# Kernel tuning notes

Hardware: AMD Instinct MI355X
Metric: run time of the kernel (lower is better)

## Reference

```python
import jax, jax.numpy as jnp
import numpy as np

TOKENS, D_MODEL, FC1, FC2 = 4096, 4096, 16384, 4096
EPS = 1e-3


def setup_inputs() -> dict:
    key = jax.random.key(0)
    ks = jax.random.split(key, 3)
    return {
        "inputs": jax.random.normal(ks[0], (TOKENS, D_MODEL), dtype=jnp.float32),
        "gamma": jnp.ones((D_MODEL,), dtype=jnp.float32),
        "beta": jnp.zeros((D_MODEL,), dtype=jnp.float32),
        "fc1_kernel": jax.random.normal(ks[1], (D_MODEL, FC1), dtype=jnp.float32) * 0.023,
        "fc1_bias": jnp.zeros((FC1,), dtype=jnp.float32),
        "fc2_kernel": jax.random.normal(ks[2], (FC1, FC2), dtype=jnp.float32) * 0.023,
        "fc2_bias": jnp.zeros((FC2,), dtype=jnp.float32),
    }


def _layernorm(x, gamma, beta):
    mu = jnp.mean(x, axis=-1, keepdims=True)
    var = jnp.mean(jnp.square(x - mu), axis=-1, keepdims=True)
    rsigma = jax.lax.rsqrt(var + EPS)
    return (x - mu) * rsigma * gamma + beta


def _gelu_tanh(x):
    # gelu with approximate=True (tanh approximation)
    c = jnp.asarray(0.7978845608028654, x.dtype)  # sqrt(2/pi)
    return 0.5 * x * (1.0 + jnp.tanh(c * (x + 0.044715 * x * x * x)))


def reference(inputs, gamma, beta, fc1_kernel, fc1_bias, fc2_kernel, fc2_bias):
    ln_out = _layernorm(inputs, gamma, beta)            # [T, D]
    fc1_out = jnp.matmul(ln_out, fc1_kernel) + fc1_bias  # [T, FC1]
    gelu_out = _gelu_tanh(fc1_out)
    fc2_out = jnp.matmul(gelu_out, fc2_kernel) + fc2_bias  # [T, FC2]
    return fc2_out
```

## Files before the change

### kernel.cpp

```cpp
#include <hip/hip_runtime.h>
#include <stdint.h>

#define TOKENS 4096
#define DMODEL 4096
#define FC1N   16384
#define FC2N   4096

typedef __attribute__((ext_vector_type(8))) __bf16 bf16x8;
typedef __attribute__((ext_vector_type(4))) float f32x4;

__device__ __forceinline__ unsigned short f2bf(float f) {
  unsigned u = __float_as_uint(f);
  u += 0x7fffu + ((u >> 16) & 1u);
  return (unsigned short)(u >> 16);
}

__device__ __forceinline__ float gelu_tanh(float x) {
  float y = 0.7978845608028654f * (x + 0.044715f * x * x * x);
  float e = __expf(2.0f * y);
  float t = 1.0f - 2.0f / (e + 1.0f);
  return 0.5f * x * (1.0f + t);
}

__global__ __launch_bounds__(256) void ln_kernel(const float* __restrict__ x,
                                                 const float* __restrict__ gamma,
                                                 const float* __restrict__ beta,
                                                 unsigned short* __restrict__ out) {
  const int row = blockIdx.x;
  const int tid = threadIdx.x;
  const float* xr = x + (size_t)row * DMODEL;
  float4 v[4];
  float s = 0.f, s2 = 0.f;
#pragma unroll
  for (int i = 0; i < 4; ++i) {
    v[i] = ((const float4*)xr)[tid + i * 256];
    s  += v[i].x + v[i].y + v[i].z + v[i].w;
    s2 += v[i].x * v[i].x + v[i].y * v[i].y + v[i].z * v[i].z + v[i].w * v[i].w;
  }
#pragma unroll
  for (int o = 32; o > 0; o >>= 1) {
    s  += __shfl_xor(s, o, 64);
    s2 += __shfl_xor(s2, o, 64);
  }
  __shared__ float red[2][4];
  const int wid = tid >> 6, lane = tid & 63;
  if (lane == 0) { red[0][wid] = s; red[1][wid] = s2; }
  __syncthreads();
  s  = red[0][0] + red[0][1] + red[0][2] + red[0][3];
  s2 = red[1][0] + red[1][1] + red[1][2] + red[1][3];
  const float mu = s * (1.f / DMODEL);
  const float var = s2 * (1.f / DMODEL) - mu * mu;
  const float rs = rsqrtf(var + 1e-3f);
  unsigned short* orow = out + (size_t)row * DMODEL;
#pragma unroll
  for (int i = 0; i < 4; ++i) {
    const int c4 = tid + i * 256;
    float4 g = ((const float4*)gamma)[c4];
    float4 b = ((const float4*)beta)[c4];
    ushort4 o;
    o.x = f2bf((v[i].x - mu) * rs * g.x + b.x);
    o.y = f2bf((v[i].y - mu) * rs * g.y + b.y);
    o.z = f2bf((v[i].z - mu) * rs * g.z + b.z);
    o.w = f2bf((v[i].w - mu) * rs * g.w + b.w);
    ((ushort4*)orow)[c4] = o;
  }
}

__global__ __launch_bounds__(256) void transpose_bf16(const float* __restrict__ W,
                                                      unsigned short* __restrict__ Wt,
                                                      int K, int N) {
  __shared__ float t[32][33];
  const int x = threadIdx.x & 31, y = threadIdx.x >> 5;
  const int n0 = blockIdx.x << 5, k0 = blockIdx.y << 5;
#pragma unroll
  for (int i = 0; i < 4; ++i)
    t[y + i * 8][x] = W[(size_t)(k0 + y + i * 8) * N + n0 + x];
  __syncthreads();
#pragma unroll
  for (int i = 0; i < 4; ++i)
    Wt[(size_t)(n0 + y + i * 8) * K + k0 + x] = f2bf(t[x][y + i * 8]);
}


template <bool GELU>
__global__ __launch_bounds__(512, 2) void gemm256(const unsigned short* __restrict__ A,
                                                  const unsigned short* __restrict__ Bt,
                                                  const float* __restrict__ bias,
                                                  void* __restrict__ Cout,
                                                  int M, int N, int K) {
  extern __shared__ char smem[];
  const int tid = threadIdx.x;
  const int lane = tid & 63, wid = tid >> 6;
  const int lane15 = lane & 15, laneHi = lane >> 4;

  const int nwg = gridDim.x;
  const int bid = blockIdx.x;
  const int cpx = nwg >> 3;
  const int wg = (bid & 7) * cpx + (bid >> 3);
  const int nbx = N >> 8;
  const int bx = wg % nbx, by = wg / nbx;
  const int m0 = by << 8, n0 = bx << 8;
  const int wr = wid >> 2, wc = wid & 3;
  const int aRow0 = (wr << 7) + lane15;
  const int bRow0 = (wc << 6) + lane15;

  const int swz = (lane15 & 7) << 4;
  const int offA0 = aRow0 * 128 + ((laneHi << 4) ^ swz);
  const int offA1 = offA0 ^ 64;
  const int offB0 = 32768 + bRow0 * 128 + ((laneHi << 4) ^ swz);
  const int offB1 = offB0 ^ 64;

  const int o0 = tid << 4, o1 = (512 + tid) << 4;
  const int r0 = o0 >> 7, r1 = o1 >> 7;
  const size_t g0 = (size_t)r0 * (K * 2) + ((o0 & 127) ^ ((r0 & 7) << 4));
  const size_t g1 = (size_t)r1 * (K * 2) + ((o1 & 127) ^ ((r1 & 7) << 4));

  const char* pAlo = (const char*)(A  + (size_t)m0 * K);
  const char* pAhi = (const char*)(A  + (size_t)(m0 + 128) * K);
  const char* pBlo = (const char*)(Bt + (size_t)n0 * K);
  const char* pBhi = (const char*)(Bt + (size_t)(n0 + 128) * K);

  auto stage = [&](const char* panel, size_t ktb, int ldsoff) {
    __builtin_amdgcn_global_load_lds(
        (const __attribute__((address_space(1))) void*)(panel + ktb + g0),
        (__attribute__((address_space(3))) void*)(smem + ldsoff + o0), 16, 0, 0);
    __builtin_amdgcn_global_load_lds(
        (const __attribute__((address_space(1))) void*)(panel + ktb + g1),
        (__attribute__((address_space(3))) void*)(smem + ldsoff + o1), 16, 0, 0);
  };
  auto rd = [&](int off) -> bf16x8 { return *(const bf16x8*)(smem + off); };

  const int NT = K >> 6;
  const int NIT = NT >> 1;

  f32x4 acc[8][4];
#pragma unroll
  for (int m = 0; m < 8; ++m)
#pragma unroll
    for (int n = 0; n < 4; ++n) acc[m][n] = f32x4{0.f, 0.f, 0.f, 0.f};

  enum { B0_ALO = 0, B0_AHI = 16384, B0_BLO = 32768, B0_BHI = 49152,
         B1_ALO = 65536, B1_AHI = 81920, B1_BLO = 98304, B1_BHI = 114688 };

  stage(pBlo, 0, B0_BLO); stage(pBhi, 0, B0_BHI);
  stage(pAlo, 0, B0_ALO); stage(pAhi, 0, B0_AHI);
  stage(pBlo, 128, B1_BLO); stage(pBhi, 128, B1_BHI);
  asm volatile("s_waitcnt vmcnt(4)" ::: "memory");
  __builtin_amdgcn_sched_barrier(0);
  __builtin_amdgcn_s_barrier();
  __builtin_amdgcn_sched_barrier(0);

  bf16x8 aL[4][2], aH[4][2], bL[2][2], bH[2][2];

#pragma unroll
  for (int n = 0; n < 2; ++n) {
    bL[n][0] = rd(offB0 + n * 2048); bL[n][1] = rd(offB1 + n * 2048);
  }

#define MFMA_Q(AF, BF, MO, NO)                                                   \
  __builtin_amdgcn_s_setprio(1);                                                 \
  _Pragma("unroll")                                                              \
  for (int ks = 0; ks < 2; ++ks)                                                 \
    _Pragma("unroll")                                                            \
    for (int m = 0; m < 4; ++m)                                                  \
      _Pragma("unroll")                                                          \
      for (int n = 0; n < 2; ++n)                                                \
        acc[m + MO][n + NO] = __builtin_amdgcn_mfma_f32_16x16x32_bf16(           \
            AF[m][ks], BF[n][ks], acc[m + MO][n + NO], 0, 0, 0);                 \
  __builtin_amdgcn_s_setprio(0);

#define RD_AL(B)                                                                 \
  _Pragma("unroll")                                                              \
  for (int m = 0; m < 4; ++m) {                                                  \
    aL[m][0] = rd(B + offA0 + m * 2048); aL[m][1] = rd(B + offA1 + m * 2048);    \
  }
#define RD_AH(B)                                                                 \
  _Pragma("unroll")                                                              \
  for (int m = 0; m < 4; ++m) {                                                  \
    aH[m][0] = rd(B + offA0 + (m + 4) * 2048);                                   \
    aH[m][1] = rd(B + offA1 + (m + 4) * 2048);                                   \
  }
#define RD_BL(B)                                                                 \
  _Pragma("unroll")                                                              \
  for (int n = 0; n < 2; ++n) {                                                  \
    bL[n][0] = rd(B + offB0 + n * 2048); bL[n][1] = rd(B + offB1 + n * 2048);    \
  }
#define RD_BH(B)                                                                 \
  _Pragma("unroll")                                                              \
  for (int n = 0; n < 2; ++n) {                                                  \
    bH[n][0] = rd(B + offB0 + (n + 2) * 2048);                                   \
    bH[n][1] = rd(B + offB1 + (n + 2) * 2048);                                   \
  }
#define BAR __builtin_amdgcn_s_barrier()
#define SB  __builtin_amdgcn_sched_barrier(0)
#define CHECK4                                                                   \
  asm volatile("s_waitcnt vmcnt(4)" ::: "memory");                               \
  SB;

  for (int it = 0; it < NIT; ++it) {
    const int u = it << 1;
    const size_t ktbV = (size_t)(u + 1) << 7;
    const int c2 = (u + 2 < NT) ? u + 2 : NT - 1;
    const int c3 = (u + 3 < NT) ? u + 3 : NT - 1;
    const size_t ktb2 = (size_t)c2 << 7, ktb3 = (size_t)c3 << 7;

    RD_AL(0) stage(pAlo, ktbV, B1_ALO);
    MFMA_Q(aL, bL, 0, 0)
    RD_BH(0) stage(pAhi, ktbV, B1_AHI);
    MFMA_Q(aL, bH, 0, 2)
    CHECK4 BAR; SB;

    RD_AH(0) stage(pBlo, ktb2, B0_BLO);
    MFMA_Q(aH, bL, 4, 0)
    RD_BL(65536) stage(pBhi, ktb2, B0_BHI);
    MFMA_Q(aH, bH, 4, 2)
    CHECK4 BAR; SB;

    RD_AL(65536) stage(pAlo, ktb2, B0_ALO);
    MFMA_Q(aL, bL, 0, 0)
    RD_BH(65536) stage(pAhi, ktb2, B0_AHI);
    MFMA_Q(aL, bH, 0, 2)
    CHECK4 BAR; SB;

    RD_AH(65536) stage(pBlo, ktb3, B1_BLO);
    MFMA_Q(aH, bL, 4, 0)
    RD_BL(0) stage(pBhi, ktb3, B1_BHI);
    MFMA_Q(aH, bH, 4, 2)
    CHECK4 BAR; SB;
  }
#undef MFMA_Q
#undef RD_AL
#undef RD_AH
#undef RD_BL
#undef RD_BH
#undef BAR
#undef SB
#undef CHECK4

  asm volatile("s_waitcnt vmcnt(0)" ::: "memory");

#pragma unroll
  for (int nf = 0; nf < 4; ++nf) {
    const int col = n0 + (wc << 6) + (nf << 4) + lane15;
    const float bs = bias[col];
#pragma unroll
    for (int mf = 0; mf < 8; ++mf) {
      const int rbase = m0 + (wr << 7) + (mf << 4) + (laneHi << 2);
#pragma unroll
      for (int j = 0; j < 4; ++j) {
        const float v = acc[mf][nf][j] + bs;
        if (GELU) {
          ((unsigned short*)Cout)[(size_t)(rbase + j) * N + col] = f2bf(gelu_tanh(v));
        } else {
          ((float*)Cout)[(size_t)(rbase + j) * N + col] = v;
        }
      }
    }
  }
}

extern "C" void kernel_launch(void* const* d_in, const int* in_sizes, int n_in,
                              void* d_out, int out_size, void* d_ws, size_t ws_size,
                              hipStream_t stream) {
  const float* x     = (const float*)d_in[0];
  const float* gamma = (const float*)d_in[1];
  const float* beta  = (const float*)d_in[2];
  const float* w1    = (const float*)d_in[3];
  const float* b1    = (const float*)d_in[4];
  const float* w2    = (const float*)d_in[5];
  const float* b2    = (const float*)d_in[6];

  unsigned short* lnout = (unsigned short*)d_ws;
  unsigned short* gout  = (unsigned short*)((char*)d_ws + (size_t)32  * 1024 * 1024);
  unsigned short* wT    = (unsigned short*)((char*)d_ws + (size_t)160 * 1024 * 1024);

  (void)hipFuncSetAttribute((const void*)gemm256<true>,
                            hipFuncAttributeMaxDynamicSharedMemorySize, 131072);
  (void)hipFuncSetAttribute((const void*)gemm256<false>,
                            hipFuncAttributeMaxDynamicSharedMemorySize, 131072);

  ln_kernel<<<TOKENS, 256, 0, stream>>>(x, gamma, beta, lnout);

  transpose_bf16<<<dim3(FC1N / 32, DMODEL / 32), 256, 0, stream>>>(w1, wT, DMODEL, FC1N);
  gemm256<true><<<dim3((TOKENS / 256) * (FC1N / 256)), 512, 131072, stream>>>(
      lnout, wT, b1, (void*)gout, TOKENS, FC1N, DMODEL);

  transpose_bf16<<<dim3(FC2N / 32, FC1N / 32), 256, 0, stream>>>(w2, wT, FC1N, FC2N);
  gemm256<false><<<dim3((TOKENS / 256) * (FC2N / 256)), 512, 131072, stream>>>(
      gout, wT, b2, d_out, TOKENS, FC2N, FC1N);
}
```

Baseline: 1.094 ms.

## Restructure GEMM LDS double-buffer pipeline to stage full tiles per half-iteration

Reorganizes the software pipeline of the bf16 MFMA GEMM. The prologue now preloads both A halves of the second buffer, and each phase issues all four global-to-LDS stages for the next tile together. Synchronization changes from vmcnt(4) checks at every barrier to full vmcnt(0) waits on alternate barriers plus lgkmcnt(0) before each barrier. The aim is to cut barrier stalls and let LDS reads run ahead of the MFMAs, at the risk of exposing global load latency through the stricter vmcnt(0) waits.

```diff
diff --git a/kernel.cpp b/kernel.cpp
--- a/kernel.cpp
+++ b/kernel.cpp
@@ -145,17 +145,13 @@
   stage(pBlo, 0, B0_BLO); stage(pBhi, 0, B0_BHI);
   stage(pAlo, 0, B0_ALO); stage(pAhi, 0, B0_AHI);
   stage(pBlo, 128, B1_BLO); stage(pBhi, 128, B1_BHI);
-  asm volatile("s_waitcnt vmcnt(4)" ::: "memory");
+  stage(pAlo, 128, B1_ALO); stage(pAhi, 128, B1_AHI);
+  asm volatile("s_waitcnt vmcnt(8)" ::: "memory");
   __builtin_amdgcn_sched_barrier(0);
   __builtin_amdgcn_s_barrier();
   __builtin_amdgcn_sched_barrier(0);
 
   bf16x8 aL[4][2], aH[4][2], bL[2][2], bH[2][2];
-
-#pragma unroll
-  for (int n = 0; n < 2; ++n) {
-    bL[n][0] = rd(offB0 + n * 2048); bL[n][1] = rd(offB1 + n * 2048);
-  }
 
 #define MFMA_Q(AF, BF, MO, NO)                                                   \
   __builtin_amdgcn_s_setprio(1);                                                 \
@@ -193,40 +189,45 @@
   }
 #define BAR __builtin_amdgcn_s_barrier()
 #define SB  __builtin_amdgcn_sched_barrier(0)
-#define CHECK4                                                                   \
-  asm volatile("s_waitcnt vmcnt(4)" ::: "memory");                               \
-  SB;
+#define LGKM0 asm volatile("s_waitcnt lgkmcnt(0)" ::: "memory")
+#define VM0   asm volatile("s_waitcnt vmcnt(0)" ::: "memory")
+
+  RD_AL(0)
+  RD_BL(0)
 
   for (int it = 0; it < NIT; ++it) {
     const int u = it << 1;
-    const size_t ktbV = (size_t)(u + 1) << 7;
     const int c2 = (u + 2 < NT) ? u + 2 : NT - 1;
     const int c3 = (u + 3 < NT) ? u + 3 : NT - 1;
     const size_t ktb2 = (size_t)c2 << 7, ktb3 = (size_t)c3 << 7;
 
-    RD_AL(0) stage(pAlo, ktbV, B1_ALO);
+    RD_BH(0)
     MFMA_Q(aL, bL, 0, 0)
-    RD_BH(0) stage(pAhi, ktbV, B1_AHI);
+    RD_AH(0)
     MFMA_Q(aL, bH, 0, 2)
-    CHECK4 BAR; SB;
-
-    RD_AH(0) stage(pBlo, ktb2, B0_BLO);
+    LGKM0; VM0;
+    SB; BAR; SB;
+
+    RD_AL(65536) stage(pBlo, ktb2, B0_BLO); stage(pAlo, ktb2, B0_ALO);
     MFMA_Q(aH, bL, 4, 0)
-    RD_BL(65536) stage(pBhi, ktb2, B0_BHI);
+    RD_BL(65536) stage(pBhi, ktb2, B0_BHI); stage(pAhi, ktb2, B0_AHI);
     MFMA_Q(aH, bH, 4, 2)
-    CHECK4 BAR; SB;
-
-    RD_AL(65536) stage(pAlo, ktb2, B0_ALO);
+    LGKM0;
+    SB; BAR; SB;
+
+    RD_BH(65536)
     MFMA_Q(aL, bL, 0, 0)
-    RD_BH(65536) stage(pAhi, ktb2, B0_AHI);
+    RD_AH(65536)
     MFMA_Q(aL, bH, 0, 2)
-    CHECK4 BAR; SB;
-
-    RD_AH(65536) stage(pBlo, ktb3, B1_BLO);
+    LGKM0; VM0;
+    SB; BAR; SB;
+
+    RD_AL(0) stage(pBlo, ktb3, B1_BLO); stage(pAlo, ktb3, B1_ALO);
     MFMA_Q(aH, bL, 4, 0)
-    RD_BL(0) stage(pBhi, ktb3, B1_BHI);
+    RD_BL(0) stage(pBhi, ktb3, B1_BHI); stage(pAhi, ktb3, B1_AHI);
     MFMA_Q(aH, bH, 4, 2)
-    CHECK4 BAR; SB;
+    LGKM0;
+    SB; BAR; SB;
   }
 #undef MFMA_Q
 #undef RD_AL
@@ -235,7 +236,8 @@
 #undef RD_BH
 #undef BAR
 #undef SB
-#undef CHECK4
+#undef LGKM0
+#undef VM0
 
   asm volatile("s_waitcnt vmcnt(0)" ::: "memory");
 
```

Measured after the change: 1.140 ms. 1.04x slower.
